# Performance work log

Hardware: AMD Instinct MI355X
Metric: run time of the kernel (lower is better)

## Reference

```python
import jax, jax.numpy as jnp
import numpy as np

EPS = 1e-6

def rmsnorm(x, w):
    v = jnp.mean(jnp.square(x), axis=-1, keepdims=True)
    return x * jax.lax.rsqrt(v + EPS) * w

def setup_inputs() -> dict:
    key = jax.random.key(0)
    ks = jax.random.split(key, 12)
    H, Di, L = 2048, 4096, 1024   # hidden, mamba inner (expand*H), seq tokens
    DT, N, K = 128, 16, 4         # dt_rank, d_state, d_conv
    F = 8192                      # MLP intermediate
    s = lambda k, shp, sc: jax.random.normal(k, shp, jnp.float32) * sc
    return dict(
        hidden_states=s(ks[0], (L, H), 1.0),
        in_ln_w=jnp.ones((H,), jnp.float32),
        pre_ff_ln_w=jnp.ones((H,), jnp.float32),
        in_proj_w=s(ks[1], (2 * Di, H), 0.02),
        conv_w=s(ks[2], (Di, K), 0.1),
        conv_b=s(ks[3], (Di,), 0.1),
        x_proj_w=s(ks[4], (DT + 2 * N, Di), 0.02),
        dt_ln_w=jnp.ones((DT,), jnp.float32),
        b_ln_w=jnp.ones((N,), jnp.float32),
        c_ln_w=jnp.ones((N,), jnp.float32),
        dt_proj_w=s(ks[5], (Di, DT), 0.02),
        dt_proj_b=s(ks[6], (Di,), 0.1),
        A=-jnp.exp(jax.random.uniform(ks[7], (Di, N), jnp.float32, -4.0, 0.0)),
        D=jnp.ones((Di,), jnp.float32),
        out_proj_w=s(ks[8], (H, Di), 0.02),
        gate_up_w=s(ks[9], (2 * F, H), 0.02),
        down_w=s(ks[10], (H, F), 0.02),
    )

def reference(hidden_states, in_ln_w, pre_ff_ln_w, in_proj_w, conv_w, conv_b,
              x_proj_w, dt_ln_w, b_ln_w, c_ln_w, dt_proj_w, dt_proj_b,
              A, D, out_proj_w, gate_up_w, down_w):
    residual = hidden_states
    x = rmsnorm(hidden_states, in_ln_w)
    # --- Mamba mixer (prefill / selective_scan path) ---
    proj = x @ in_proj_w.T                          # [L, 2*Di]
    Di = in_proj_w.shape[0] // 2
    h, gate = proj[:, :Di], proj[:, Di:]
    # causal depthwise conv1d, kernel K, left pad K-1, then silu
    K = conv_w.shape[1]
    L = h.shape[0]
    hp = jnp.pad(h, ((K - 1, 0), (0, 0)))           # [L+K-1, Di]
    idx = jnp.arange(L)[:, None] + jnp.arange(K)[None, :]
    h = jnp.einsum('lkd,dk->ld', hp[idx], conv_w) + conv_b
    h = jax.nn.silu(h)
    # ssm parameters
    ssm = h @ x_proj_w.T                            # [L, DT+2N]
    DTr = dt_ln_w.shape[0]
    N = b_ln_w.shape[0]
    dt = rmsnorm(ssm[:, :DTr], dt_ln_w)
    B = rmsnorm(ssm[:, DTr:DTr + N], b_ln_w)
    C = rmsnorm(ssm[:, DTr + N:], c_ln_w)
    delta = jax.nn.softplus(dt @ dt_proj_w.T + dt_proj_b)   # [L, Di]
    # selective scan (discretize then linear recurrence over L)
    dA = jnp.exp(delta[:, :, None] * A[None, :, :])         # [L, Di, N]
    dBu = delta[:, :, None] * B[:, None, :] * h[:, :, None] # [L, Di, N]
    def step(s, inp):
        da, dbu = inp
        s = da * s + dbu
        return s, s
    s0 = jnp.zeros((Di, N), jnp.float32)
    _, states = jax.lax.scan(step, s0, (dA, dBu))           # [L, Di, N]
    y = jnp.einsum('ldn,ln->ld', states, C) + h * D
    y = y * jax.nn.silu(gate)
    mixer_out = y @ out_proj_w.T                    # [L, H]
    # --- residual + pre-FF norm + gated MLP ---
    residual = residual + mixer_out
    x = rmsnorm(residual, pre_ff_ln_w)
    gu = x @ gate_up_w.T                            # [L, 2F]
    F = down_w.shape[1]
    x = jax.nn.silu(gu[:, :F]) * gu[:, F:]
    ff = x @ down_w.T
    return residual + ff
```

## Files before the change

### kernel.cpp

```cpp
#include <hip/hip_runtime.h>
#include <math.h>

typedef unsigned short u16;
typedef __bf16 bf16x8 __attribute__((ext_vector_type(8)));
typedef short s16x8 __attribute__((ext_vector_type(8)));
typedef short s16x4 __attribute__((ext_vector_type(4)));
typedef float f32x4 __attribute__((ext_vector_type(4)));

__device__ __forceinline__ u16 f2bf(float f) {
  union { float f; unsigned u; } v; v.f = f;
  unsigned u = v.u;
  unsigned r = u + 0x7fffu + ((u >> 16) & 1u);
  return (u16)(r >> 16);
}
__device__ __forceinline__ float bf2f(u16 h) {
  union { unsigned u; float f; } v; v.u = ((unsigned)h) << 16;
  return v.f;
}
__device__ __forceinline__ float fast_softplus(float x) {
  return (x > 20.f) ? x : __logf(1.f + __expf(x));
}
__device__ __forceinline__ float fast_sig(float x) {
  return __builtin_amdgcn_rcpf(1.f + __expf(-x));
}

__device__ __forceinline__ void gld_lds16(const u16* g, u16* l) {
  __builtin_amdgcn_global_load_lds(
      (const __attribute__((address_space(1))) unsigned int*)g,
      (__attribute__((address_space(3))) unsigned int*)l, 16, 0, 0);
}

__global__ __launch_bounds__(256)
void f32_to_bf16_k(const float* __restrict__ src, u16* __restrict__ dst,
                   int n, int n_valid) {
  int i = (blockIdx.x * 256 + threadIdx.x) * 4;
  if (i >= n) return;
  s16x4 o;
  if (i + 3 < n_valid) {
    float4 v = *(const float4*)(src + i);
    o[0] = (short)f2bf(v.x); o[1] = (short)f2bf(v.y);
    o[2] = (short)f2bf(v.z); o[3] = (short)f2bf(v.w);
  } else {
    o[0] = 0; o[1] = 0; o[2] = 0; o[3] = 0;
  }
  *(s16x4*)(dst + i) = o;
}

template <int BN, int MODE>
__global__ __launch_bounds__(256)
void gemm2(const u16* __restrict__ A, const u16* __restrict__ B,
           float* __restrict__ C, u16* __restrict__ Cb,
           const u16* __restrict__ aux, int M, int Nc, int K) {
  constexpr int NJ = BN / 32;
  constexpr int BISS = BN / 32;
  __shared__ __align__(16) u16 As[64 * 64];
  __shared__ __align__(16) u16 Bs[BN * 64];
  const int tid = threadIdx.x;
  const int tm0 = blockIdx.y * 64;
  const int tn0 = blockIdx.x * BN;
  const int wave = tid >> 6;
  const int lane = tid & 63;
  const int wm = (wave >> 1) * 32;
  const int wn = (wave & 1) * (BN / 2);
  const int frow = lane & 15;
  const int fc = lane >> 4;
  const int rmask = frow & 7;

  const int r0 = tid >> 3;
  const int csw = (((tid & 7) ^ (r0 & 7)) << 3);
  const u16* gA = A + (size_t)(tm0 + r0) * K + csw;
  const u16* gB = B + (size_t)(tn0 + r0) * K + csw;
  u16* lA = &As[tid * 8];
  u16* lB = &Bs[tid * 8];

  f32x4 acc[2][NJ];
  f32x4 zero = {0.f, 0.f, 0.f, 0.f};
#pragma unroll
  for (int i = 0; i < 2; ++i)
#pragma unroll
    for (int j = 0; j < NJ; ++j) acc[i][j] = zero;

  for (int kt = 0; kt < K; kt += 64) {
    __syncthreads();
    gld_lds16(gA, lA);
    gld_lds16(gA + (size_t)32 * K, lA + 2048);
#pragma unroll
    for (int b = 0; b < BISS; ++b)
      gld_lds16(gB + (size_t)32 * b * K, lB + b * 2048);
    gA += 64; gB += 64;
    __syncthreads();
#pragma unroll
    for (int s = 0; s < 2; ++s) {
      bf16x8 af[2], bfr[NJ];
#pragma unroll
      for (int i = 0; i < 2; ++i) {
        int addr = (wm + i * 16 + frow) * 64 + (((s * 4 + fc) ^ rmask) << 3);
        af[i] = __builtin_bit_cast(bf16x8, *(const s16x8*)&As[addr]);
      }
#pragma unroll
      for (int j = 0; j < NJ; ++j) {
        int addr = (wn + j * 16 + frow) * 64 + (((s * 4 + fc) ^ rmask) << 3);
        bfr[j] = __builtin_bit_cast(bf16x8, *(const s16x8*)&Bs[addr]);
      }
#pragma unroll
      for (int i = 0; i < 2; ++i)
#pragma unroll
        for (int j = 0; j < NJ; ++j)
          acc[i][j] = __builtin_amdgcn_mfma_f32_16x16x32_bf16(af[i], bfr[j], acc[i][j], 0, 0, 0);
    }
  }
  const int ccol = lane & 15;
  const int crow = (lane >> 4) * 4;
#pragma unroll
  for (int i = 0; i < 2; ++i) {
#pragma unroll
    for (int j = 0; j < NJ; ++j) {
      int gn = tn0 + wn + j * 16 + ccol;
      if (gn < Nc) {
        size_t base = (size_t)(tm0 + wm + i * 16 + crow) * Nc + gn;
#pragma unroll
        for (int r = 0; r < 4; ++r) {
          float c = acc[i][j][r];
          size_t idx = base + (size_t)r * Nc;
          if (MODE == 0) {
            C[idx] = c;
          } else if (MODE == 1) {
            Cb[idx] = f2bf(c * fast_sig(c));
          } else {
            Cb[idx] = f2bf(c * bf2f(aux[idx]));
          }
        }
      }
    }
  }
}

__device__ inline float block_reduce_sum_256(float v) {
  __shared__ float red[4];
  int lane = threadIdx.x & 63, wave = threadIdx.x >> 6;
#pragma unroll
  for (int m = 32; m > 0; m >>= 1) v += __shfl_xor(v, m, 64);
  if (lane == 0) red[wave] = v;
  __syncthreads();
  return red[0] + red[1] + red[2] + red[3];
}

__global__ __launch_bounds__(256)
void rmsnorm2048_k(const float* __restrict__ x, const float* __restrict__ w,
                   u16* __restrict__ y) {
  const int C = 2048;
  const int row = blockIdx.x;
  const int t = threadIdx.x;
  const float4* xr = (const float4*)(x + (size_t)row * C);
  float4 v0 = xr[t];
  float4 v1 = xr[t + 256];
  float ss = v0.x * v0.x + v0.y * v0.y + v0.z * v0.z + v0.w * v0.w +
             v1.x * v1.x + v1.y * v1.y + v1.z * v1.z + v1.w * v1.w;
  float tot = block_reduce_sum_256(ss);
  float sc = rsqrtf(tot * (1.0f / C) + 1e-6f);
  const float4* wr = (const float4*)w;
  float4 w0 = wr[t], w1 = wr[t + 256];
  u16* yr = y + (size_t)row * C;
  s16x4 o0, o1;
  o0[0] = (short)f2bf(v0.x * sc * w0.x); o0[1] = (short)f2bf(v0.y * sc * w0.y);
  o0[2] = (short)f2bf(v0.z * sc * w0.z); o0[3] = (short)f2bf(v0.w * sc * w0.w);
  o1[0] = (short)f2bf(v1.x * sc * w1.x); o1[1] = (short)f2bf(v1.y * sc * w1.y);
  o1[2] = (short)f2bf(v1.z * sc * w1.z); o1[3] = (short)f2bf(v1.w * sc * w1.w);
  *(s16x4*)(yr + t * 4) = o0;
  *(s16x4*)(yr + 1024 + t * 4) = o1;
}

__global__ __launch_bounds__(256)
void add_rmsnorm_k(const float* __restrict__ a, const float* __restrict__ b,
                   const float* __restrict__ w, float* __restrict__ resid,
                   u16* __restrict__ y) {
  const int C = 2048;
  const int row = blockIdx.x;
  const int t = threadIdx.x;
  const float4* ar = (const float4*)(a + (size_t)row * C);
  const float4* br = (const float4*)(b + (size_t)row * C);
  float4 v0 = ar[t], v1 = ar[t + 256];
  float4 u0 = br[t], u1 = br[t + 256];
  v0.x += u0.x; v0.y += u0.y; v0.z += u0.z; v0.w += u0.w;
  v1.x += u1.x; v1.y += u1.y; v1.z += u1.z; v1.w += u1.w;
  float4* rr = (float4*)(resid + (size_t)row * C);
  rr[t] = v0; rr[t + 256] = v1;
  float ss = v0.x * v0.x + v0.y * v0.y + v0.z * v0.z + v0.w * v0.w +
             v1.x * v1.x + v1.y * v1.y + v1.z * v1.z + v1.w * v1.w;
  float tot = block_reduce_sum_256(ss);
  float sc = rsqrtf(tot * (1.0f / C) + 1e-6f);
  const float4* wr = (const float4*)w;
  float4 w0 = wr[t], w1 = wr[t + 256];
  u16* yr = y + (size_t)row * C;
  s16x4 o0, o1;
  o0[0] = (short)f2bf(v0.x * sc * w0.x); o0[1] = (short)f2bf(v0.y * sc * w0.y);
  o0[2] = (short)f2bf(v0.z * sc * w0.z); o0[3] = (short)f2bf(v0.w * sc * w0.w);
  o1[0] = (short)f2bf(v1.x * sc * w1.x); o1[1] = (short)f2bf(v1.y * sc * w1.y);
  o1[2] = (short)f2bf(v1.z * sc * w1.z); o1[3] = (short)f2bf(v1.w * sc * w1.w);
  *(s16x4*)(yr + t * 4) = o0;
  *(s16x4*)(yr + 1024 + t * 4) = o1;
}

__global__ __launch_bounds__(256)
void conv_silu_k(const float* __restrict__ proj, const float* __restrict__ cw,
                 const float* __restrict__ cb, u16* __restrict__ h) {
  const int Di = 4096, LD = 8192;
  int idx = blockIdx.x * 256 + threadIdx.x;
  int d = idx & (Di - 1);
  int l = idx >> 12;
  float4 w = *(const float4*)(cw + (size_t)d * 4);
  float acc = cb[d];
  int ls0 = l - 3;
  if (ls0 >= 0) acc += proj[(size_t)ls0 * LD + d] * w.x;
  if (ls0 + 1 >= 0) acc += proj[(size_t)(ls0 + 1) * LD + d] * w.y;
  if (ls0 + 2 >= 0) acc += proj[(size_t)(ls0 + 2) * LD + d] * w.z;
  acc += proj[(size_t)l * LD + d] * w.w;
  h[idx] = f2bf(acc * fast_sig(acc));
}

__global__ __launch_bounds__(64)
void ssm_norm_k(const float* __restrict__ ssm, const float* __restrict__ dtw,
                const float* __restrict__ bw, const float* __restrict__ cw,
                u16* __restrict__ dtn, float* __restrict__ Bn,
                float* __restrict__ Cn) {
  int l = blockIdx.x;
  int lane = threadIdx.x;
  const float* r = ssm + (size_t)l * 160;
  float d0 = r[lane];
  float d1 = r[lane + 64];
  float bv = (lane < 16) ? r[128 + lane] : 0.f;
  float cv = (lane < 16) ? r[144 + lane] : 0.f;
  float sd = d0 * d0 + d1 * d1;
  float sb = bv * bv;
  float sc = cv * cv;
#pragma unroll
  for (int m = 32; m > 0; m >>= 1) {
    sd += __shfl_xor(sd, m, 64);
    sb += __shfl_xor(sb, m, 64);
    sc += __shfl_xor(sc, m, 64);
  }
  float scd = rsqrtf(sd * (1.f / 128.f) + 1e-6f);
  float scb = rsqrtf(sb * (1.f / 16.f) + 1e-6f);
  float scc = rsqrtf(sc * (1.f / 16.f) + 1e-6f);
  dtn[(size_t)l * 128 + lane] = f2bf(d0 * scd * dtw[lane]);
  dtn[(size_t)l * 128 + lane + 64] = f2bf(d1 * scd * dtw[lane + 64]);
  if (lane < 16) {
    Bn[(size_t)l * 16 + lane] = bv * scb * bw[lane];
    Cn[(size_t)l * 16 + lane] = cv * scc * cw[lane];
  }
}

#define NCH 32
#define CHL 32

__global__ __launch_bounds__(256)
void scan_p1(const float* __restrict__ dpre, const float* __restrict__ dtb,
             const u16* __restrict__ h, const float* __restrict__ Bn,
             const float* __restrict__ Amat,
             float* __restrict__ carryA, float* __restrict__ carryS) {
  const int Di = 4096;
  int chunk = blockIdx.x & (NCH - 1);
  int d = (blockIdx.x >> 5) * 256 + threadIdx.x;
  __shared__ float Bs[CHL * 16];
  for (int i = threadIdx.x; i < CHL * 16; i += 256)
    Bs[i] = Bn[(size_t)chunk * CHL * 16 + i];
  __syncthreads();
  float a[16];
#pragma unroll
  for (int q = 0; q < 4; ++q)
    *(float4*)&a[q * 4] = *(const float4*)(Amat + (size_t)d * 16 + q * 4);
  float bias = dtb[d];
  float s[16];
#pragma unroll
  for (int n = 0; n < 16; ++n) s[n] = 0.f;
  float sumdel = 0.f;
  int l0 = chunk * CHL;
#pragma unroll 4
  for (int j = 0; j < CHL; ++j) {
    int l = l0 + j;
    float del = fast_softplus(dpre[(size_t)l * Di + d] + bias);
    float hv = bf2f(h[(size_t)l * Di + d]);
    sumdel += del;
    float c = del * hv;
#pragma unroll
    for (int n = 0; n < 16; ++n) {
      float dA = __expf(del * a[n]);
      s[n] = dA * s[n] + c * Bs[j * 16 + n];
    }
  }
  size_t base = (size_t)chunk * 65536 + (size_t)d * 16;
#pragma unroll
  for (int n = 0; n < 16; ++n) {
    carryA[base + n] = __expf(sumdel * a[n]);
    carryS[base + n] = s[n];
  }
}

__global__ __launch_bounds__(256)
void scan_p2(const float* __restrict__ carryA, float* __restrict__ carryS) {
  int p = blockIdx.x * 256 + threadIdx.x;
  float cin = 0.f;
#pragma unroll
  for (int c = 0; c < NCH; ++c) {
    float av = carryA[(size_t)c * 65536 + p];
    float sv = carryS[(size_t)c * 65536 + p];
    float nx = av * cin + sv;
    carryS[(size_t)c * 65536 + p] = cin;
    cin = nx;
  }
}

__global__ __launch_bounds__(256)
void scan_p3(const float* __restrict__ dpre, const float* __restrict__ dtb,
             const u16* __restrict__ h, const float* __restrict__ Bn,
             const float* __restrict__ Cn, const float* __restrict__ Amat,
             const float* __restrict__ Dw, const float* __restrict__ proj,
             const float* __restrict__ carryS, u16* __restrict__ y) {
  const int Di = 4096;
  int chunk = blockIdx.x & (NCH - 1);
  int d = (blockIdx.x >> 5) * 256 + threadIdx.x;
  __shared__ float Bs[CHL * 16];
  __shared__ float Cs[CHL * 16];
  for (int i = threadIdx.x; i < CHL * 16; i += 256) {
    Bs[i] = Bn[(size_t)chunk * CHL * 16 + i];
    Cs[i] = Cn[(size_t)chunk * CHL * 16 + i];
  }
  __syncthreads();
  float a[16];
#pragma unroll
  for (int q = 0; q < 4; ++q)
    *(float4*)&a[q * 4] = *(const float4*)(Amat + (size_t)d * 16 + q * 4);
  float bias = dtb[d];
  float Dd = Dw[d];
  float s[16];
  size_t base = (size_t)chunk * 65536 + (size_t)d * 16;
#pragma unroll
  for (int q = 0; q < 4; ++q)
    *(float4*)&s[q * 4] = *(const float4*)(carryS + base + q * 4);
  int l0 = chunk * CHL;
#pragma unroll 2
  for (int j = 0; j < CHL; ++j) {
    int l = l0 + j;
    float del = fast_softplus(dpre[(size_t)l * Di + d] + bias);
    float hv = bf2f(h[(size_t)l * Di + d]);
    float c = del * hv;
    float p = 0.f;
#pragma unroll
    for (int n = 0; n < 16; ++n) {
      float dA = __expf(del * a[n]);
      s[n] = dA * s[n] + c * Bs[j * 16 + n];
      p += s[n] * Cs[j * 16 + n];
    }
    float g = proj[(size_t)l * 8192 + 4096 + d];
    float yv = p + hv * Dd;
    y[(size_t)l * Di + d] = f2bf(yv * g * fast_sig(g));
  }
}

__global__ __launch_bounds__(256)
void add_k(float* __restrict__ out, const float* __restrict__ ff) {
  int i = blockIdx.x * 256 + threadIdx.x;
  float4 a = ((const float4*)out)[i];
  float4 b = ((const float4*)ff)[i];
  a.x += b.x; a.y += b.y; a.z += b.z; a.w += b.w;
  ((float4*)out)[i] = a;
}

extern "C" void kernel_launch(void* const* d_in, const int* in_sizes, int n_in,
                              void* d_out, int out_size, void* d_ws, size_t ws_size,
                              hipStream_t stream) {
  const float* hidden      = (const float*)d_in[0];
  const float* in_ln_w     = (const float*)d_in[1];
  const float* pre_ff_ln_w = (const float*)d_in[2];
  const float* in_proj_w   = (const float*)d_in[3];
  const float* conv_w      = (const float*)d_in[4];
  const float* conv_b      = (const float*)d_in[5];
  const float* x_proj_w    = (const float*)d_in[6];
  const float* dt_ln_w     = (const float*)d_in[7];
  const float* b_ln_w      = (const float*)d_in[8];
  const float* c_ln_w      = (const float*)d_in[9];
  const float* dt_proj_w   = (const float*)d_in[10];
  const float* dt_proj_b   = (const float*)d_in[11];
  const float* Amat        = (const float*)d_in[12];
  const float* Dw          = (const float*)d_in[13];
  const float* out_proj_w  = (const float*)d_in[14];
  const float* gate_up_w   = (const float*)d_in[15];
  const float* down_w      = (const float*)d_in[16];
  float* out = (float*)d_out;
  float* ws = (float*)d_ws;

  const int L = 1024, H = 2048, Di = 4096, F = 8192;

  u16*   wbuf   = (u16*)ws;
  float* carryA = ws + 2097152;
  float* carryS = ws + 4194304;
  float* proj   = ws + 8388608;
  float* dpre   = ws + 16777216;
  u16*   hbuf   = (u16*)(ws + 20971520);
  u16*   xnorm  = (u16*)(ws + 23068672);
  float* ssm    = ws + 24117248;
  u16*   dtn    = (u16*)(ws + 24281088);
  float* Bn     = ws + 24346624;
  float* Cn     = ws + 24363008;
  u16*   ybuf   = (u16*)(ws + 24379392);
  float* mix    = ws + 16777216;
  u16*   x2     = (u16*)(ws + 18874368);
  u16*   sg     = (u16*)(ws + 8388608);
  u16*   x3     = (u16*)(ws + 12582912);
  float* ff     = ws + 19922944;

  rmsnorm2048_k<<<L, 256, 0, stream>>>(hidden, in_ln_w, xnorm);
  f32_to_bf16_k<<<16384, 256, 0, stream>>>(in_proj_w, wbuf, 16777216, 16777216);
  gemm2<128, 0><<<dim3(64, 16), 256, 0, stream>>>(xnorm, wbuf, proj, nullptr, nullptr, L, 8192, 2048);
  conv_silu_k<<<(L * Di) / 256, 256, 0, stream>>>(proj, conv_w, conv_b, hbuf);
  f32_to_bf16_k<<<1024, 256, 0, stream>>>(x_proj_w, wbuf, 1048576, 655360);
  gemm2<64, 0><<<dim3(4, 16), 256, 0, stream>>>(hbuf, wbuf, ssm, nullptr, nullptr, L, 160, 4096);
  ssm_norm_k<<<L, 64, 0, stream>>>(ssm, dt_ln_w, b_ln_w, c_ln_w, dtn, Bn, Cn);
  f32_to_bf16_k<<<512, 256, 0, stream>>>(dt_proj_w, wbuf, 524288, 524288);
  gemm2<128, 0><<<dim3(32, 16), 256, 0, stream>>>(dtn, wbuf, dpre, nullptr, nullptr, L, 4096, 128);
  scan_p1<<<16 * NCH, 256, 0, stream>>>(dpre, dt_proj_b, hbuf, Bn, Amat, carryA, carryS);
  scan_p2<<<256, 256, 0, stream>>>(carryA, carryS);
  scan_p3<<<16 * NCH, 256, 0, stream>>>(dpre, dt_proj_b, hbuf, Bn, Cn, Amat, Dw, proj, carryS, ybuf);
  f32_to_bf16_k<<<8192, 256, 0, stream>>>(out_proj_w, wbuf, 8388608, 8388608);
  gemm2<64, 0><<<dim3(32, 16), 256, 0, stream>>>(ybuf, wbuf, mix, nullptr, nullptr, L, 2048, 4096);
  add_rmsnorm_k<<<L, 256, 0, stream>>>(hidden, mix, pre_ff_ln_w, out, x2);
  f32_to_bf16_k<<<16384, 256, 0, stream>>>(gate_up_w, wbuf, 16777216, 16777216);
  gemm2<128, 1><<<dim3(64, 16), 256, 0, stream>>>(x2, wbuf, nullptr, sg, nullptr, L, 8192, 2048);
  f32_to_bf16_k<<<16384, 256, 0, stream>>>(gate_up_w + 16777216, wbuf, 16777216, 16777216);
  gemm2<128, 2><<<dim3(64, 16), 256, 0, stream>>>(x2, wbuf, nullptr, x3, sg, L, 8192, 2048);
  f32_to_bf16_k<<<16384, 256, 0, stream>>>(down_w, wbuf, 16777216, 16777216);
  gemm2<64, 0><<<dim3(32, 16), 256, 0, stream>>>(x3, wbuf, ff, nullptr, nullptr, L, 2048, 8192);
  add_k<<<(L * H / 4) / 256, 256, 0, stream>>>(out, ff);
}
```

Before: 726.6 us.

## Load GEMM B-fragments directly from global into registers with double buffering

Replaces the GEMM kernel with a variant that no longer stages the weight (B) tile in shared memory. Each lane loads its B fragments straight from global memory into a two-deep register buffer, prefetching two k-steps ahead. Only A goes through LDS, now with a larger K block of 256 so there are fewer barriers. A launch-bounds occupancy hint of 4 is added. This trades LDS traffic and syncs for uncoalesced-ish direct global loads of B and more register pressure.

New measurement: 1.050 ms. 44.5% more time.

```diff
diff --git a/kernel.cpp b/kernel.cpp
--- a/kernel.cpp
+++ b/kernel.cpp
@@ -46,15 +46,15 @@
   *(s16x4*)(dst + i) = o;
 }
 
-template <int BN, int MODE>
-__global__ __launch_bounds__(256)
-void gemm2(const u16* __restrict__ A, const u16* __restrict__ B,
+template <int NJ, int KB, int MODE>
+__global__ __launch_bounds__(256, 4)
+void gemm3(const u16* __restrict__ A, const u16* __restrict__ B,
            float* __restrict__ C, u16* __restrict__ Cb,
            const u16* __restrict__ aux, int M, int Nc, int K) {
-  constexpr int NJ = BN / 32;
-  constexpr int BISS = BN / 32;
-  __shared__ __align__(16) u16 As[64 * 64];
-  __shared__ __align__(16) u16 Bs[BN * 64];
+  constexpr int BN = NJ * 32;
+  constexpr int NSUB = KB / 64;
+  constexpr int NSS = KB / 32;
+  __shared__ __align__(16) u16 As[64 * KB];
   const int tid = threadIdx.x;
   const int tm0 = blockIdx.y * 64;
   const int tn0 = blockIdx.x * BN;
@@ -69,9 +69,12 @@
   const int r0 = tid >> 3;
   const int csw = (((tid & 7) ^ (r0 & 7)) << 3);
   const u16* gA = A + (size_t)(tm0 + r0) * K + csw;
-  const u16* gB = B + (size_t)(tn0 + r0) * K + csw;
   u16* lA = &As[tid * 8];
-  u16* lB = &Bs[tid * 8];
+
+  const u16* gBr[NJ];
+#pragma unroll
+  for (int j = 0; j < NJ; ++j)
+    gBr[j] = B + (size_t)(tn0 + wn + j * 16 + frow) * K + fc * 8;
 
   f32x4 acc[2][NJ];
   f32x4 zero = {0.f, 0.f, 0.f, 0.f};
@@ -80,33 +83,44 @@
 #pragma unroll
     for (int j = 0; j < NJ; ++j) acc[i][j] = zero;
 
-  for (int kt = 0; kt < K; kt += 64) {
+  const int S = K / 32;
+  s16x8 bbuf[2][NJ];
+#pragma unroll
+  for (int p = 0; p < 2; ++p)
+#pragma unroll
+    for (int j = 0; j < NJ; ++j)
+      bbuf[p][j] = *(const s16x8*)(gBr[j] + p * 32);
+
+  for (int kt = 0; kt < K; kt += KB) {
     __syncthreads();
-    gld_lds16(gA, lA);
-    gld_lds16(gA + (size_t)32 * K, lA + 2048);
-#pragma unroll
-    for (int b = 0; b < BISS; ++b)
-      gld_lds16(gB + (size_t)32 * b * K, lB + b * 2048);
-    gA += 64; gB += 64;
+#pragma unroll
+    for (int q = 0; q < NSUB; ++q) {
+      gld_lds16(gA + kt + q * 64, lA + q * 4096);
+      gld_lds16(gA + (size_t)32 * K + kt + q * 64, lA + q * 4096 + 2048);
+    }
     __syncthreads();
 #pragma unroll
-    for (int s = 0; s < 2; ++s) {
-      bf16x8 af[2], bfr[NJ];
+    for (int s = 0; s < NSS; ++s) {
+      const int fs = (kt >> 5) + s;
+      const int p = fs & 1;
+      bf16x8 af[2];
 #pragma unroll
       for (int i = 0; i < 2; ++i) {
-        int addr = (wm + i * 16 + frow) * 64 + (((s * 4 + fc) ^ rmask) << 3);
+        int addr = (s >> 1) * 4096 + (wm + i * 16 + frow) * 64 +
+                   ((((s & 1) * 4 + fc) ^ rmask) << 3);
         af[i] = __builtin_bit_cast(bf16x8, *(const s16x8*)&As[addr]);
       }
 #pragma unroll
-      for (int j = 0; j < NJ; ++j) {
-        int addr = (wn + j * 16 + frow) * 64 + (((s * 4 + fc) ^ rmask) << 3);
-        bfr[j] = __builtin_bit_cast(bf16x8, *(const s16x8*)&Bs[addr]);
+      for (int i = 0; i < 2; ++i)
+#pragma unroll
+        for (int j = 0; j < NJ; ++j)
+          acc[i][j] = __builtin_amdgcn_mfma_f32_16x16x32_bf16(
+              af[i], __builtin_bit_cast(bf16x8, bbuf[p][j]), acc[i][j], 0, 0, 0);
+      if (fs + 2 < S) {
+#pragma unroll
+        for (int j = 0; j < NJ; ++j)
+          bbuf[p][j] = *(const s16x8*)(gBr[j] + (fs + 2) * 32);
       }
-#pragma unroll
-      for (int i = 0; i < 2; ++i)
-#pragma unroll
-        for (int j = 0; j < NJ; ++j)
-          acc[i][j] = __builtin_amdgcn_mfma_f32_16x16x32_bf16(af[i], bfr[j], acc[i][j], 0, 0, 0);
     }
   }
   const int ccol = lane & 15;
@@ -411,24 +425,24 @@
 
   rmsnorm2048_k<<<L, 256, 0, stream>>>(hidden, in_ln_w, xnorm);
   f32_to_bf16_k<<<16384, 256, 0, stream>>>(in_proj_w, wbuf, 16777216, 16777216);
-  gemm2<128, 0><<<dim3(64, 16), 256, 0, stream>>>(xnorm, wbuf, proj, nullptr, nullptr, L, 8192, 2048);
+  gemm3<4, 256, 0><<<dim3(64, 16), 256, 0, stream>>>(xnorm, wbuf, proj, nullptr, nullptr, L, 8192, 2048);
   conv_silu_k<<<(L * Di) / 256, 256, 0, stream>>>(proj, conv_w, conv_b, hbuf);
   f32_to_bf16_k<<<1024, 256, 0, stream>>>(x_proj_w, wbuf, 1048576, 655360);
-  gemm2<64, 0><<<dim3(4, 16), 256, 0, stream>>>(hbuf, wbuf, ssm, nullptr, nullptr, L, 160, 4096);
+  gemm3<2, 256, 0><<<dim3(4, 16), 256, 0, stream>>>(hbuf, wbuf, ssm, nullptr, nullptr, L, 160, 4096);
   ssm_norm_k<<<L, 64, 0, stream>>>(ssm, dt_ln_w, b_ln_w, c_ln_w, dtn, Bn, Cn);
   f32_to_bf16_k<<<512, 256, 0, stream>>>(dt_proj_w, wbuf, 524288, 524288);
-  gemm2<128, 0><<<dim3(32, 16), 256, 0, stream>>>(dtn, wbuf, dpre, nullptr, nullptr, L, 4096, 128);
+  gemm3<4, 128, 0><<<dim3(32, 16), 256, 0, stream>>>(dtn, wbuf, dpre, nullptr, nullptr, L, 4096, 128);
   scan_p1<<<16 * NCH, 256, 0, stream>>>(dpre, dt_proj_b, hbuf, Bn, Amat, carryA, carryS);
   scan_p2<<<256, 256, 0, stream>>>(carryA, carryS);
   scan_p3<<<16 * NCH, 256, 0, stream>>>(dpre, dt_proj_b, hbuf, Bn, Cn, Amat, Dw, proj, carryS, ybuf);
   f32_to_bf16_k<<<8192, 256, 0, stream>>>(out_proj_w, wbuf, 8388608, 8388608);
-  gemm2<64, 0><<<dim3(32, 16), 256, 0, stream>>>(ybuf, wbuf, mix, nullptr, nullptr, L, 2048, 4096);
+  gemm3<2, 256, 0><<<dim3(32, 16), 256, 0, stream>>>(ybuf, wbuf, mix, nullptr, nullptr, L, 2048, 4096);
   add_rmsnorm_k<<<L, 256, 0, stream>>>(hidden, mix, pre_ff_ln_w, out, x2);
   f32_to_bf16_k<<<16384, 256, 0, stream>>>(gate_up_w, wbuf, 16777216, 16777216);
-  gemm2<128, 1><<<dim3(64, 16), 256, 0, stream>>>(x2, wbuf, nullptr, sg, nullptr, L, 8192, 2048);
+  gemm3<4, 256, 1><<<dim3(64, 16), 256, 0, stream>>>(x2, wbuf, nullptr, sg, nullptr, L, 8192, 2048);
   f32_to_bf16_k<<<16384, 256, 0, stream>>>(gate_up_w + 16777216, wbuf, 16777216, 16777216);
-  gemm2<128, 2><<<dim3(64, 16), 256, 0, stream>>>(x2, wbuf, nullptr, x3, sg, L, 8192, 2048);
+  gemm3<4, 256, 2><<<dim3(64, 16), 256, 0, stream>>>(x2, wbuf, nullptr, x3, sg, L, 8192, 2048);
   f32_to_bf16_k<<<16384, 256, 0, stream>>>(down_w, wbuf, 16777216, 16777216);
-  gemm2<64, 0><<<dim3(32, 16), 256, 0, stream>>>(x3, wbuf, ff, nullptr, nullptr, L, 2048, 8192);
+  gemm3<2, 256, 0><<<dim3(32, 16), 256, 0, stream>>>(x3, wbuf, ff, nullptr, nullptr, L, 2048, 8192);
   add_k<<<(L * H / 4) / 256, 256, 0, stream>>>(out, ff);
 }
```
